# Kernel tuning notes

Measured on AMD Instinct MI355X. Metric: run time of the kernel, lower is better.

The kernel has to match this reference:

```python
import jax, jax.numpy as jnp
import numpy as np

N_NODES = 20000
DIM = 128
N_EDGES = 500000
BATCH = 16384
EPS = 1e-6  # torch.nn.PairwiseDistance default eps


def setup_inputs() -> dict:
    key = jax.random.key(0)
    k = jax.random.split(key, 8)
    edges = jax.random.randint(k[0], (2, N_EDGES), 0, N_NODES, dtype=jnp.int64 if jax.config.jax_enable_x64 else jnp.int32)
    nodes_p_star = jnp.sort(jax.random.randint(k[1], (BATCH,), 0, N_NODES))
    nodes_p = jnp.sort(jax.random.randint(k[2], (BATCH,), 0, N_NODES))
    # learned parameters, init in [-1, 1) as in the torch module
    beta_p = 2.0 * jax.random.uniform(k[3], (N_NODES,), dtype=jnp.float32) - 1.0
    beta_p_star = 2.0 * jax.random.uniform(k[4], (N_NODES,), dtype=jnp.float32) - 1.0
    p = 2.0 * jax.random.uniform(k[5], (N_NODES, DIM), dtype=jnp.float32) - 1.0
    p_star = 2.0 * jax.random.uniform(k[6], (N_NODES, DIM), dtype=jnp.float32) - 1.0
    return {
        "edges": edges,
        "nodes_p_star": nodes_p_star,
        "nodes_p": nodes_p,
        "beta_p": beta_p,
        "beta_p_star": beta_p_star,
        "p": p,
        "p_star": p_star,
    }


def reference(edges, nodes_p_star, nodes_p, beta_p, beta_p_star, p, p_star):
    # ---- link term: sum over observed edges of (beta - dist) ----
    beta_pair = beta_p_star[edges[0]] + beta_p[edges[1]]  # [E]
    diff = p[edges[0]] - p_star[edges[1]]                 # [E, D]
    # torch PairwiseDistance adds eps to the difference before the norm
    z_dist = jnp.sqrt(jnp.sum((diff + EPS) ** 2, axis=-1))
    link_term = jnp.sum(beta_pair - z_dist)

    # ---- non-link term: triu-masked sum of exp(beta - cdist) ----
    bps = beta_p_star[nodes_p_star]   # [Ns]
    bp = beta_p[nodes_p]              # [Np]
    ps = p_star[nodes_p_star]         # [Ns, D]
    pp = p[nodes_p]                   # [Np, D]
    beta_mat = bps[None, :] + bp[:, None]          # [Np, Ns]
    # cdist(ps, pp) -> [Ns, Np] via Gram trick
    sq = (jnp.sum(ps * ps, axis=-1)[:, None]
          + jnp.sum(pp * pp, axis=-1)[None, :]
          - 2.0 * jnp.einsum('nd,md->nm', ps, pp))
    dist_mat = jnp.sqrt(jnp.maximum(sq, 0.0))      # [Ns, Np]
    intensity = jnp.exp(beta_mat.T - dist_mat)     # [Ns, Np]
    non_link = jnp.sum(jnp.triu(intensity, k=1))

    return -(link_term - non_link)
```

## Files before the change

kernel.cpp:

```cpp
#include <hip/hip_runtime.h>

#define N_NODES 20000
#define DIM 128
#define N_EDGES 500000
#define BATCH 16384
#define EPS 1e-6f
#define L2E 1.4426950408889634f

typedef _Float16 half8 __attribute__((ext_vector_type(8)));
typedef _Float16 half4_t __attribute__((ext_vector_type(4)));
typedef float f32x4 __attribute__((ext_vector_type(4)));

__device__ __forceinline__ float fast_sqrtf(float x) {
#if __has_builtin(__builtin_amdgcn_sqrtf)
    return __builtin_amdgcn_sqrtf(x);
#else
    return sqrtf(x);
#endif
}
__device__ __forceinline__ float fast_exp2f(float x) {
#if __has_builtin(__builtin_amdgcn_exp2f)
    return __builtin_amdgcn_exp2f(x);
#else
    return exp2f(x);
#endif
}

#define NB_TILE 8256
#define N_BLK   512

#define OFF_PGEMM 0
#define OFF_CTR   16384
#define OFF_PSH   33280
#define OFF_PPH   4227584
#define OFF_N2S   8421888
#define OFF_N2P   8487424
#define OFF_BPS   8552960
#define OFF_BP    8618496
#define OFF_END   8684032

__global__ __launch_bounds__(256) void prep_kernel(
    const float* __restrict__ p, const float* __restrict__ p_star,
    const float* __restrict__ beta_p, const float* __restrict__ beta_ps,
    const int* __restrict__ nodes_ps, const int* __restrict__ nodes_p,
    _Float16* __restrict__ Ah, float* __restrict__ n2A, float* __restrict__ bA2,
    _Float16* __restrict__ Bh, float* __restrict__ n2B, float* __restrict__ bB2,
    unsigned* __restrict__ ctr)
{
    if (blockIdx.x == 0 && threadIdx.x == 0) *ctr = 0u;
    const int bx = blockIdx.x;
    const int g = threadIdx.x & 31;
    const int r8 = threadIdx.x >> 5;
    const bool isA = bx < 2048;
    const int row = (isA ? bx : bx - 2048) * 8 + r8;
    const int id = isA ? nodes_ps[row] : nodes_p[row];
    const float* src = isA ? p_star : p;
    float4 v = ((const float4*)(src + (size_t)id * DIM))[g];
    half4_t o;
    o[0] = (_Float16)v.x; o[1] = (_Float16)v.y; o[2] = (_Float16)v.z; o[3] = (_Float16)v.w;
    const int h = g >> 4;
    const int pc = ((g >> 1) & 7) ^ (row & 7);
    _Float16* dst = isA ? Ah : Bh;
    *(half4_t*)(dst + (size_t)row * DIM + (((h << 3) | pc) << 3) + (g & 1) * 4) = o;
    float nrm = v.x * v.x + v.y * v.y + v.z * v.z + v.w * v.w;
    #pragma unroll
    for (int m = 16; m >= 1; m >>= 1) nrm += __shfl_xor(nrm, m, 32);
    if (g == 0) {
        if (isA) { n2A[row] = nrm; bA2[row] = L2E * beta_ps[id]; }
        else     { n2B[row] = nrm; bB2[row] = L2E * beta_p[id]; }
    }
}

__device__ __forceinline__ void tile_of(int t, int& i0, int& j0, bool& diag) {
    const int by = t / 129;
    const int bx = t - by * 129;
    const int len = 128 - by;
    int ti, tj;
    if (bx < len) { ti = by; tj = by + bx; }
    else          { ti = 127 - by; tj = 127 - (bx - len); }
    i0 = ti << 7; j0 = tj << 7; diag = (ti == tj);
}

#define STAGE_ARR(BASE0, GSRC, LDSOFF)                                             \
    {                                                                              \
        _Pragma("unroll")                                                          \
        for (int u = 0; u < 4; ++u) {                                              \
            const int g8 = u * 8 + w;                                   \
            const int h = g8 >> 4, rg = g8 & 15;                                   \
            __builtin_amdgcn_global_load_lds(                                      \
                (const __attribute__((address_space(1))) void*)((GSRC) +           \
                    (((size_t)((BASE0) + rg * 8 + (lane >> 3))) << 8)              \
                    + (h << 7) + ((lane & 7) << 4)),                               \
                (__attribute__((address_space(3))) void*)(lds + (LDSOFF)           \
                    + h * 16384 + rg * 1024), 16, 0, 0);                           \
        }                                                                          \
    }

#define STAGE_A(I0) STAGE_ARR(I0, gA, 0)
#define STAGE_B(J0) STAGE_ARR(J0, gB, 32768)

__global__ __launch_bounds__(512, 4) void main_kernel(
    const _Float16* __restrict__ Ag, const _Float16* __restrict__ Bg,
    const float* __restrict__ n2A, const float* __restrict__ n2B,
    const float* __restrict__ bA2, const float* __restrict__ bB2,
    const int* __restrict__ edges,
    const float* __restrict__ beta_p, const float* __restrict__ beta_ps,
    const float* __restrict__ pf, const float* __restrict__ psf,
    float* __restrict__ pgemm, unsigned* __restrict__ ctr,
    float* __restrict__ out)
{
    __shared__ __align__(16) _Float16 sm16[32768];
    __shared__ float smr[8];
    __shared__ int lastflag;

    const int b = blockIdx.x;
    const int tid = threadIdx.x;
    const int lane = tid & 63;
    const int w = tid >> 6;
    const int wm = w & 3;
    const int wn = w >> 2;
    const int quad = lane >> 4;
    const int lr = lane & 15;
    const int k7 = lr & 7;

    auto* lds = (__attribute__((address_space(3))) char*)sm16;
    const auto* gA = (const __attribute__((address_space(1))) char*)Ag;
    const auto* gB = (const __attribute__((address_space(1))) char*)Bg;

    float lsum = 0.f;

    const int start = b * 16 + (b < 64 ? b : 64);
    const int tend = start + 16 + (b < 64 ? 1 : 0);

    int t = start;
    int i0, j0; bool diag;
    tile_of(t, i0, j0, diag);
    STAGE_A(i0)
    STAGE_B(j0)
    __syncthreads();

    for (;;) {
        int cls = 0;
        if (diag) cls = (wn == 0) ? (wm >= 2 ? 2 : 1) : (wm >= 2 ? 1 : 0);

        f32x4 acc[2][4] = {};
        if (cls != 2) {
            #pragma unroll
            for (int ks = 0; ks < 4; ++ks) {
                const int h = ks >> 1;
                const int pc = (((ks & 1) << 2) | quad) ^ k7;
                const int hb = h * 8192;
                half8 af[2], bf[4];
                #pragma unroll
                for (int u = 0; u < 2; ++u)
                    af[u] = *(const half8*)&sm16[hb + (wm * 32 + u * 16 + lr) * 64 + pc * 8];
                #pragma unroll
                for (int v = 0; v < 4; ++v)
                    bf[v] = *(const half8*)&sm16[16384 + hb + (wn * 64 + v * 16 + lr) * 64 + pc * 8];
                #pragma unroll
                for (int mi = 0; mi < 2; ++mi)
                    #pragma unroll
                    for (int ni = 0; ni < 4; ++ni)
                        acc[mi][ni] = __builtin_amdgcn_mfma_f32_16x16x32_f16(
                            af[mi], bf[ni], acc[mi][ni], 0, 0, 0);
            }
        }

        const int ilo = i0 + wm * 32, jlo = j0 + wn * 64;
        const int tcur = t;
        __syncthreads();

        t += 1;
        const bool more = (t < tend);
        if (more) {
            const int pi0 = i0;
            tile_of(t, i0, j0, diag);
            if (i0 != pi0) STAGE_A(i0)
            STAGE_B(j0)
        }

        #pragma unroll
        for (int tt = 0; tt < 2; ++tt) {
            int e = tcur * 64 + w * 8 + quad * 2 + tt;
            if (e < N_EDGES) {
                int e0 = edges[e];
                int e1 = edges[N_EDGES + e];
                const float* ar = pf + (size_t)e0 * DIM + lr * 8;
                const float* br = psf + (size_t)e1 * DIM + lr * 8;
                f32x4 a0 = *(const f32x4*)ar;   f32x4 a1 = *(const f32x4*)(ar + 4);
                f32x4 b0 = *(const f32x4*)br;   f32x4 b1 = *(const f32x4*)(br + 4);
                float eb2 = (lr == 0) ? (beta_ps[e0] + beta_p[e1]) : 0.f;
                float s = 0.f;
                #pragma unroll
                for (int k = 0; k < 4; ++k) { float d = a0[k] - b0[k] + EPS; s = fmaf(d, d, s); }
                #pragma unroll
                for (int k = 0; k < 4; ++k) { float d = a1[k] - b1[k] + EPS; s = fmaf(d, d, s); }
                #pragma unroll
                for (int m = 8; m >= 1; m >>= 1) s += __shfl_xor(s, m, 16);
                if (lr == 0) lsum -= eb2 - fast_sqrtf(s);
            }
        }

        if (cls != 2) {
            f32x4 n2i[2], bi[2];
            #pragma unroll
            for (int mi = 0; mi < 2; ++mi) {
                n2i[mi] = *(const f32x4*)&n2A[ilo + mi * 16 + quad * 4];
                bi[mi]  = *(const f32x4*)&bA2[ilo + mi * 16 + quad * 4];
            }
            float n2j[4], bj[4];
            #pragma unroll
            for (int ni = 0; ni < 4; ++ni) {
                n2j[ni] = n2B[jlo + ni * 16 + lr];
                bj[ni]  = bB2[jlo + ni * 16 + lr];
            }

            if (cls == 0) {
                #pragma unroll
                for (int mi = 0; mi < 2; ++mi)
                    #pragma unroll
                    for (int ni = 0; ni < 4; ++ni) {
                        f32x4 d = acc[mi][ni];
                        f32x4 ttv = n2i[mi] + n2j[ni];
                        f32x4 sq = d * -2.0f + ttv;
                        f32x4 bs = bi[mi] + bj[ni];
                        #pragma unroll
                        for (int r = 0; r < 4; ++r) {
                            float m0 = fmaxf(sq[r], 0.f);
                            float arg = fmaf(fast_sqrtf(m0), -L2E, bs[r]);
                            lsum += fast_exp2f(arg);
                        }
                    }
            } else {
                #pragma unroll
                for (int mi = 0; mi < 2; ++mi)
                    #pragma unroll
                    for (int ni = 0; ni < 4; ++ni) {
                        f32x4 d = acc[mi][ni];
                        f32x4 ttv = n2i[mi] + n2j[ni];
                        f32x4 sq = d * -2.0f + ttv;
                        f32x4 bs = bi[mi] + bj[ni];
                        #pragma unroll
                        for (int r = 0; r < 4; ++r) {
                            int ig = ilo + mi * 16 + quad * 4 + r;
                            int jg = jlo + ni * 16 + lr;
                            float m0 = fmaxf(sq[r], 0.f);
                            float arg = fmaf(fast_sqrtf(m0), -L2E, bs[r]);
                            float ex = fast_exp2f(arg);
                            if (jg > ig) lsum += ex;
                        }
                    }
            }
        }

        if (!more) break;
        __syncthreads();
    }

    #pragma unroll
    for (int m = 32; m >= 1; m >>= 1) lsum += __shfl_xor(lsum, m, 64);
    if (lane == 0) smr[w] = lsum;
    __syncthreads();
    if (tid == 0) {
        float s = 0.f;
        #pragma unroll
        for (int i = 0; i < 8; ++i) s += smr[i];
        pgemm[b] = s;
        unsigned prev = __hip_atomic_fetch_add(ctr, 1u, __ATOMIC_ACQ_REL,
                                               __HIP_MEMORY_SCOPE_AGENT);
        lastflag = (prev == N_BLK - 1) ? 1 : 0;
    }
    __syncthreads();

    if (lastflag) {
        float s = __hip_atomic_load(&pgemm[tid], __ATOMIC_RELAXED,
                                    __HIP_MEMORY_SCOPE_AGENT);
        #pragma unroll
        for (int m = 32; m >= 1; m >>= 1) s += __shfl_xor(s, m, 64);
        if (lane == 0) smr[w] = s;
        __syncthreads();
        if (tid == 0) {
            float tsum = 0.f;
            #pragma unroll
            for (int i = 0; i < 8; ++i) tsum += smr[i];
            out[0] = tsum;
        }
    }
}

extern "C" void kernel_launch(void* const* d_in, const int* in_sizes, int n_in,
                              void* d_out, int out_size, void* d_ws, size_t ws_size,
                              hipStream_t stream) {
    const int* edges = (const int*)d_in[0];
    const int* nodes_p_star = (const int*)d_in[1];
    const int* nodes_p = (const int*)d_in[2];
    const float* beta_p = (const float*)d_in[3];
    const float* beta_p_star = (const float*)d_in[4];
    const float* p = (const float*)d_in[5];
    const float* p_star = (const float*)d_in[6];

    char* ws = (char*)d_ws;
    float* pgemm = (float*)(ws + OFF_PGEMM);
    unsigned* ctr = (unsigned*)(ws + OFF_CTR);
    _Float16* psh = (_Float16*)(ws + OFF_PSH);
    _Float16* pph = (_Float16*)(ws + OFF_PPH);
    float* n2s = (float*)(ws + OFF_N2S);
    float* n2p = (float*)(ws + OFF_N2P);
    float* bps2 = (float*)(ws + OFF_BPS);
    float* bp2 = (float*)(ws + OFF_BP);

    prep_kernel<<<4096, 256, 0, stream>>>(
        p, p_star, beta_p, beta_p_star, nodes_p_star, nodes_p,
        psh, n2s, bps2, pph, n2p, bp2, ctr);

    main_kernel<<<N_BLK, 512, 0, stream>>>(
        psh, pph, n2s, n2p, bps2, bp2,
        edges, beta_p, beta_p_star, p, p_star,
        pgemm, ctr, (float*)d_out);
}
```

Baseline: 194.4 us.

## Halve B tile to 64 columns, raise occupancy, and pack epilogue math in float2

Each 128x128 tile is split into two 128x64 half-steps. This halves the B staging in LDS (48KB instead of 64KB) and the per-wave accumulator count, and lets launch bounds rise from 4 to 6 blocks per CU. Each step now processes half as many edges, so the total edge coverage is unchanged. The exp/sqrt epilogue is rewritten to use two-wide float vectors with a vector accumulator, aiming at packed FP32 ops. In exchange there are more barriers and more B reloads per A tile, and each wave has less MFMA work to hide latency.

```diff
diff --git a/kernel.cpp b/kernel.cpp
--- a/kernel.cpp
+++ b/kernel.cpp
@@ -10,6 +10,7 @@
 typedef _Float16 half8 __attribute__((ext_vector_type(8)));
 typedef _Float16 half4_t __attribute__((ext_vector_type(4)));
 typedef float f32x4 __attribute__((ext_vector_type(4)));
+typedef float f32x2 __attribute__((ext_vector_type(2)));
 
 __device__ __forceinline__ float fast_sqrtf(float x) {
 #if __has_builtin(__builtin_amdgcn_sqrtf)
@@ -27,6 +28,7 @@
 }
 
 #define NB_TILE 8256
+#define NB_STEP 16512
 #define N_BLK   512
 
 #define OFF_PGEMM 0
@@ -71,35 +73,47 @@
     }
 }
 
-__device__ __forceinline__ void tile_of(int t, int& i0, int& j0, bool& diag) {
+__device__ __forceinline__ void tile_of(int t, int& i0, int& tjb, bool& diag) {
     const int by = t / 129;
     const int bx = t - by * 129;
     const int len = 128 - by;
     int ti, tj;
     if (bx < len) { ti = by; tj = by + bx; }
     else          { ti = 127 - by; tj = 127 - (bx - len); }
-    i0 = ti << 7; j0 = tj << 7; diag = (ti == tj);
-}
-
-#define STAGE_ARR(BASE0, GSRC, LDSOFF)                                             \
+    i0 = ti << 7; tjb = tj << 7; diag = (ti == tj);
+}
+
+#define STAGE_A(I0)                                                                \
     {                                                                              \
         _Pragma("unroll")                                                          \
         for (int u = 0; u < 4; ++u) {                                              \
             const int g8 = u * 8 + w;                                   \
             const int h = g8 >> 4, rg = g8 & 15;                                   \
             __builtin_amdgcn_global_load_lds(                                      \
-                (const __attribute__((address_space(1))) void*)((GSRC) +           \
-                    (((size_t)((BASE0) + rg * 8 + (lane >> 3))) << 8)              \
+                (const __attribute__((address_space(1))) void*)(gA +               \
+                    (((size_t)((I0) + rg * 8 + (lane >> 3))) << 8)                 \
                     + (h << 7) + ((lane & 7) << 4)),                               \
-                (__attribute__((address_space(3))) void*)(lds + (LDSOFF)           \
+                (__attribute__((address_space(3))) void*)(lds                      \
                     + h * 16384 + rg * 1024), 16, 0, 0);                           \
         }                                                                          \
     }
 
-#define STAGE_A(I0) STAGE_ARR(I0, gA, 0)
-#define STAGE_B(J0) STAGE_ARR(J0, gB, 32768)
-
-__global__ __launch_bounds__(512, 4) void main_kernel(
+#define STAGE_B(JB)                                                                \
+    {                                                                              \
+        _Pragma("unroll")                                                          \
+        for (int u = 0; u < 2; ++u) {                                              \
+            const int g8 = u * 8 + w;                                   \
+            const int h = g8 >> 3, rg = g8 & 7;                                    \
+            __builtin_amdgcn_global_load_lds(                                      \
+                (const __attribute__((address_space(1))) void*)(gB +               \
+                    (((size_t)((JB) + rg * 8 + (lane >> 3))) << 8)                 \
+                    + (h << 7) + ((lane & 7) << 4)),                               \
+                (__attribute__((address_space(3))) void*)(lds + 32768              \
+                    + h * 8192 + rg * 1024), 16, 0, 0);                            \
+        }                                                                          \
+    }
+
+__global__ __launch_bounds__(512, 6) void main_kernel(
     const _Float16* __restrict__ Ag, const _Float16* __restrict__ Bg,
     const float* __restrict__ n2A, const float* __restrict__ n2B,
     const float* __restrict__ bA2, const float* __restrict__ bB2,
@@ -109,7 +123,7 @@
     float* __restrict__ pgemm, unsigned* __restrict__ ctr,
     float* __restrict__ out)
 {
-    __shared__ __align__(16) _Float16 sm16[32768];
+    __shared__ __align__(16) _Float16 sm16[24576];
     __shared__ float smr[8];
     __shared__ int lastflag;
 
@@ -128,60 +142,65 @@
     const auto* gB = (const __attribute__((address_space(1))) char*)Bg;
 
     float lsum = 0.f;
-
-    const int start = b * 16 + (b < 64 ? b : 64);
-    const int tend = start + 16 + (b < 64 ? 1 : 0);
-
-    int t = start;
-    int i0, j0; bool diag;
-    tile_of(t, i0, j0, diag);
-    STAGE_A(i0)
-    STAGE_B(j0)
+    f32x2 lacc = {0.f, 0.f};
+
+    const int start = b * 32 + (b < 128 ? b : 128);
+    const int tend = start + 32 + (b < 128 ? 1 : 0);
+
+    int s = start;
+    int i0, tjb; bool diag;
+    {
+        tile_of(s >> 1, i0, tjb, diag);
+        const int hb = s & 1;
+        STAGE_A(i0)
+        STAGE_B(tjb + hb * 64)
+    }
     __syncthreads();
 
     for (;;) {
+        const int hb = s & 1;
         int cls = 0;
-        if (diag) cls = (wn == 0) ? (wm >= 2 ? 2 : 1) : (wm >= 2 ? 1 : 0);
-
-        f32x4 acc[2][4] = {};
+        if (diag) { const int cj = hb * 2 + wn; cls = (cj > wm) ? 0 : (cj == wm ? 1 : 2); }
+
+        f32x4 acc[2][2] = {};
         if (cls != 2) {
             #pragma unroll
             for (int ks = 0; ks < 4; ++ks) {
                 const int h = ks >> 1;
                 const int pc = (((ks & 1) << 2) | quad) ^ k7;
-                const int hb = h * 8192;
-                half8 af[2], bf[4];
+                half8 af[2], bf[2];
                 #pragma unroll
                 for (int u = 0; u < 2; ++u)
-                    af[u] = *(const half8*)&sm16[hb + (wm * 32 + u * 16 + lr) * 64 + pc * 8];
-                #pragma unroll
-                for (int v = 0; v < 4; ++v)
-                    bf[v] = *(const half8*)&sm16[16384 + hb + (wn * 64 + v * 16 + lr) * 64 + pc * 8];
+                    af[u] = *(const half8*)&sm16[h * 8192 + (wm * 32 + u * 16 + lr) * 64 + pc * 8];
+                #pragma unroll
+                for (int v = 0; v < 2; ++v)
+                    bf[v] = *(const half8*)&sm16[16384 + h * 4096 + (wn * 32 + v * 16 + lr) * 64 + pc * 8];
                 #pragma unroll
                 for (int mi = 0; mi < 2; ++mi)
                     #pragma unroll
-                    for (int ni = 0; ni < 4; ++ni)
+                    for (int ni = 0; ni < 2; ++ni)
                         acc[mi][ni] = __builtin_amdgcn_mfma_f32_16x16x32_f16(
                             af[mi], bf[ni], acc[mi][ni], 0, 0, 0);
             }
         }
 
-        const int ilo = i0 + wm * 32, jlo = j0 + wn * 64;
-        const int tcur = t;
+        const int ilo = i0 + wm * 32;
+        const int jlo = tjb + hb * 64 + wn * 32;
+        const int scur = s;
         __syncthreads();
 
-        t += 1;
-        const bool more = (t < tend);
+        s += 1;
+        const bool more = (s < tend);
         if (more) {
             const int pi0 = i0;
-            tile_of(t, i0, j0, diag);
+            tile_of(s >> 1, i0, tjb, diag);
             if (i0 != pi0) STAGE_A(i0)
-            STAGE_B(j0)
+            STAGE_B(tjb + (s & 1) * 64)
         }
 
         #pragma unroll
-        for (int tt = 0; tt < 2; ++tt) {
-            int e = tcur * 64 + w * 8 + quad * 2 + tt;
+        for (int tt = 0; tt < 1; ++tt) {
+            int e = scur * 32 + w * 4 + quad;
             if (e < N_EDGES) {
                 int e0 = edges[e];
                 int e1 = edges[N_EDGES + e];
@@ -190,14 +209,14 @@
                 f32x4 a0 = *(const f32x4*)ar;   f32x4 a1 = *(const f32x4*)(ar + 4);
                 f32x4 b0 = *(const f32x4*)br;   f32x4 b1 = *(const f32x4*)(br + 4);
                 float eb2 = (lr == 0) ? (beta_ps[e0] + beta_p[e1]) : 0.f;
-                float s = 0.f;
-                #pragma unroll
-                for (int k = 0; k < 4; ++k) { float d = a0[k] - b0[k] + EPS; s = fmaf(d, d, s); }
-                #pragma unroll
-                for (int k = 0; k < 4; ++k) { float d = a1[k] - b1[k] + EPS; s = fmaf(d, d, s); }
-                #pragma unroll
-                for (int m = 8; m >= 1; m >>= 1) s += __shfl_xor(s, m, 16);
-                if (lr == 0) lsum -= eb2 - fast_sqrtf(s);
+                float ssum = 0.f;
+                #pragma unroll
+                for (int k = 0; k < 4; ++k) { float d = a0[k] - b0[k] + EPS; ssum = fmaf(d, d, ssum); }
+                #pragma unroll
+                for (int k = 0; k < 4; ++k) { float d = a1[k] - b1[k] + EPS; ssum = fmaf(d, d, ssum); }
+                #pragma unroll
+                for (int m = 8; m >= 1; m >>= 1) ssum += __shfl_xor(ssum, m, 16);
+                if (lr == 0) lsum -= eb2 - fast_sqrtf(ssum);
             }
         }
 
@@ -208,64 +227,59 @@
                 n2i[mi] = *(const f32x4*)&n2A[ilo + mi * 16 + quad * 4];
                 bi[mi]  = *(const f32x4*)&bA2[ilo + mi * 16 + quad * 4];
             }
-            float n2j[4], bj[4];
-            #pragma unroll
-            for (int ni = 0; ni < 4; ++ni) {
+            float n2j[2], bj[2];
+            #pragma unroll
+            for (int ni = 0; ni < 2; ++ni) {
                 n2j[ni] = n2B[jlo + ni * 16 + lr];
                 bj[ni]  = bB2[jlo + ni * 16 + lr];
             }
 
-            if (cls == 0) {
-                #pragma unroll
-                for (int mi = 0; mi < 2; ++mi)
+            #pragma unroll
+            for (int mi = 0; mi < 2; ++mi)
+                #pragma unroll
+                for (int ni = 0; ni < 2; ++ni) {
+                    const f32x4 d = acc[mi][ni];
                     #pragma unroll
-                    for (int ni = 0; ni < 4; ++ni) {
-                        f32x4 d = acc[mi][ni];
-                        f32x4 ttv = n2i[mi] + n2j[ni];
-                        f32x4 sq = d * -2.0f + ttv;
-                        f32x4 bs = bi[mi] + bj[ni];
-                        #pragma unroll
-                        for (int r = 0; r < 4; ++r) {
-                            float m0 = fmaxf(sq[r], 0.f);
-                            float arg = fmaf(fast_sqrtf(m0), -L2E, bs[r]);
-                            lsum += fast_exp2f(arg);
+                    for (int pr = 0; pr < 2; ++pr) {
+                        f32x2 d2 = { d[2 * pr], d[2 * pr + 1] };
+                        f32x2 t2 = { n2i[mi][2 * pr] + n2j[ni], n2i[mi][2 * pr + 1] + n2j[ni] };
+                        f32x2 sq2 = d2 * -2.0f + t2;
+                        f32x2 z2 = { 0.f, 0.f };
+                        f32x2 mx2 = __builtin_elementwise_max(sq2, z2);
+                        float s0 = fast_sqrtf(mx2[0]);
+                        float s1 = fast_sqrtf(mx2[1]);
+                        f32x2 bs2 = { bi[mi][2 * pr] + bj[ni], bi[mi][2 * pr + 1] + bj[ni] };
+                        f32x2 sr2 = { s0, s1 };
+                        f32x2 ar2 = sr2 * -L2E + bs2;
+                        float e0 = fast_exp2f(ar2[0]);
+                        float e1 = fast_exp2f(ar2[1]);
+                        if (cls == 0) {
+                            f32x2 e2 = { e0, e1 };
+                            lacc += e2;
+                        } else {
+                            const int ig0 = ilo + mi * 16 + quad * 4 + 2 * pr;
+                            const int jg = jlo + ni * 16 + lr;
+                            if (jg > ig0)     lacc[0] += e0;
+                            if (jg > ig0 + 1) lacc[1] += e1;
                         }
                     }
-            } else {
-                #pragma unroll
-                for (int mi = 0; mi < 2; ++mi)
-                    #pragma unroll
-                    for (int ni = 0; ni < 4; ++ni) {
-                        f32x4 d = acc[mi][ni];
-                        f32x4 ttv = n2i[mi] + n2j[ni];
-                        f32x4 sq = d * -2.0f + ttv;
-                        f32x4 bs = bi[mi] + bj[ni];
-                        #pragma unroll
-                        for (int r = 0; r < 4; ++r) {
-                            int ig = ilo + mi * 16 + quad * 4 + r;
-                            int jg = jlo + ni * 16 + lr;
-                            float m0 = fmaxf(sq[r], 0.f);
-                            float arg = fmaf(fast_sqrtf(m0), -L2E, bs[r]);
-                            float ex = fast_exp2f(arg);
-                            if (jg > ig) lsum += ex;
-                        }
-                    }
-            }
+                }
         }
 
         if (!more) break;
         __syncthreads();
     }
 
+    lsum += lacc[0] + lacc[1];
     #pragma unroll
     for (int m = 32; m >= 1; m >>= 1) lsum += __shfl_xor(lsum, m, 64);
     if (lane == 0) smr[w] = lsum;
     __syncthreads();
     if (tid == 0) {
-        float s = 0.f;
+        float ssum = 0.f;
         #pragma unroll
-        for (int i = 0; i < 8; ++i) s += smr[i];
-        pgemm[b] = s;
+        for (int i = 0; i < 8; ++i) ssum += smr[i];
+        pgemm[b] = ssum;
         unsigned prev = __hip_atomic_fetch_add(ctr, 1u, __ATOMIC_ACQ_REL,
                                                __HIP_MEMORY_SCOPE_AGENT);
         lastflag = (prev == N_BLK - 1) ? 1 : 0;
@@ -273,11 +287,11 @@
     __syncthreads();
 
     if (lastflag) {
-        float s = __hip_atomic_load(&pgemm[tid], __ATOMIC_RELAXED,
+        float v = __hip_atomic_load(&pgemm[tid], __ATOMIC_RELAXED,
                                     __HIP_MEMORY_SCOPE_AGENT);
         #pragma unroll
-        for (int m = 32; m >= 1; m >>= 1) s += __shfl_xor(s, m, 64);
-        if (lane == 0) smr[w] = s;
+        for (int m = 32; m >= 1; m >>= 1) v += __shfl_xor(v, m, 64);
+        if (lane == 0) smr[w] = v;
         __syncthreads();
         if (tid == 0) {
             float tsum = 0.f;
```

Result: slower. 208.4 us (+7.3%).

## Convert full embedding tables to fp16 and prefetch edge gathers before MFMA

Applied to the files above, without the earlier changes.

The prep kernel now also converts the full p and p_star tables to fp16, and when the workspace is large enough the edge term gathers half8 rows instead of fp32, halving the gather bytes. Edge indices and rows are loaded at the top of each tile iteration so their latency overlaps the MFMA work. Row norms and betas for the A tile are hoisted and reloaded only when the A tile changes, and the block-to-tile-run mapping is interleaved by b&7. The cost is an extra pass over both 20000x128 tables in prep, fp16 rounding in the link-distance term, and more live registers during the MFMA loop.

```diff
diff --git a/kernel.cpp b/kernel.cpp
--- a/kernel.cpp
+++ b/kernel.cpp
@@ -37,7 +37,9 @@
 #define OFF_N2P   8487424
 #define OFF_BPS   8552960
 #define OFF_BP    8618496
-#define OFF_END   8684032
+#define OFF_P16   8684032
+#define OFF_PS16  13804032
+#define OFF_END   18924032
 
 __global__ __launch_bounds__(256) void prep_kernel(
     const float* __restrict__ p, const float* __restrict__ p_star,
@@ -45,29 +47,41 @@
     const int* __restrict__ nodes_ps, const int* __restrict__ nodes_p,
     _Float16* __restrict__ Ah, float* __restrict__ n2A, float* __restrict__ bA2,
     _Float16* __restrict__ Bh, float* __restrict__ n2B, float* __restrict__ bB2,
+    _Float16* __restrict__ p16, _Float16* __restrict__ ps16,
     unsigned* __restrict__ ctr)
 {
     if (blockIdx.x == 0 && threadIdx.x == 0) *ctr = 0u;
     const int bx = blockIdx.x;
     const int g = threadIdx.x & 31;
     const int r8 = threadIdx.x >> 5;
-    const bool isA = bx < 2048;
-    const int row = (isA ? bx : bx - 2048) * 8 + r8;
-    const int id = isA ? nodes_ps[row] : nodes_p[row];
-    const float* src = isA ? p_star : p;
-    float4 v = ((const float4*)(src + (size_t)id * DIM))[g];
-    half4_t o;
-    o[0] = (_Float16)v.x; o[1] = (_Float16)v.y; o[2] = (_Float16)v.z; o[3] = (_Float16)v.w;
-    const int h = g >> 4;
-    const int pc = ((g >> 1) & 7) ^ (row & 7);
-    _Float16* dst = isA ? Ah : Bh;
-    *(half4_t*)(dst + (size_t)row * DIM + (((h << 3) | pc) << 3) + (g & 1) * 4) = o;
-    float nrm = v.x * v.x + v.y * v.y + v.z * v.z + v.w * v.w;
-    #pragma unroll
-    for (int m = 16; m >= 1; m >>= 1) nrm += __shfl_xor(nrm, m, 32);
-    if (g == 0) {
-        if (isA) { n2A[row] = nrm; bA2[row] = L2E * beta_ps[id]; }
-        else     { n2B[row] = nrm; bB2[row] = L2E * beta_p[id]; }
+    if (bx < 4096) {
+        const bool isA = bx < 2048;
+        const int row = (isA ? bx : bx - 2048) * 8 + r8;
+        const int id = isA ? nodes_ps[row] : nodes_p[row];
+        const float* src = isA ? p_star : p;
+        float4 v = ((const float4*)(src + (size_t)id * DIM))[g];
+        half4_t o;
+        o[0] = (_Float16)v.x; o[1] = (_Float16)v.y; o[2] = (_Float16)v.z; o[3] = (_Float16)v.w;
+        const int h = g >> 4;
+        const int pc = ((g >> 1) & 7) ^ (row & 7);
+        _Float16* dst = isA ? Ah : Bh;
+        *(half4_t*)(dst + (size_t)row * DIM + (((h << 3) | pc) << 3) + (g & 1) * 4) = o;
+        float nrm = v.x * v.x + v.y * v.y + v.z * v.z + v.w * v.w;
+        #pragma unroll
+        for (int m = 16; m >= 1; m >>= 1) nrm += __shfl_xor(nrm, m, 32);
+        if (g == 0) {
+            if (isA) { n2A[row] = nrm; bA2[row] = L2E * beta_ps[id]; }
+            else     { n2B[row] = nrm; bB2[row] = L2E * beta_p[id]; }
+        }
+    } else {
+        const bool isP = bx < 6596;
+        const int row = (isP ? bx - 4096 : bx - 6596) * 8 + r8;
+        const float* src = isP ? p : p_star;
+        _Float16* dst = isP ? p16 : ps16;
+        float4 v = ((const float4*)(src + (size_t)row * DIM))[g];
+        half4_t o;
+        o[0] = (_Float16)v.x; o[1] = (_Float16)v.y; o[2] = (_Float16)v.z; o[3] = (_Float16)v.w;
+        *(half4_t*)(dst + (size_t)row * DIM + g * 4) = o;
     }
 }
 
@@ -81,7 +95,7 @@
     i0 = ti << 7; j0 = tj << 7; diag = (ti == tj);
 }
 
-#define STAGE_ARR(BASE0, GSRC, LDSOFF)                                             \
+#define STAGE_ARR(BASE0, GSRC, LOFF)                                               \
     {                                                                              \
         _Pragma("unroll")                                                          \
         for (int u = 0; u < 4; ++u) {                                              \
@@ -91,7 +105,7 @@
                 (const __attribute__((address_space(1))) void*)((GSRC) +           \
                     (((size_t)((BASE0) + rg * 8 + (lane >> 3))) << 8)              \
                     + (h << 7) + ((lane & 7) << 4)),                               \
-                (__attribute__((address_space(3))) void*)(lds + (LDSOFF)           \
+                (__attribute__((address_space(3))) void*)(lds + (LOFF)             \
                     + h * 16384 + rg * 1024), 16, 0, 0);                           \
         }                                                                          \
     }
@@ -105,7 +119,8 @@
     const float* __restrict__ bA2, const float* __restrict__ bB2,
     const int* __restrict__ edges,
     const float* __restrict__ beta_p, const float* __restrict__ beta_ps,
-    const float* __restrict__ pf, const float* __restrict__ psf,
+    const _Float16* __restrict__ p16, const _Float16* __restrict__ ps16,
+    const float* __restrict__ pf, const float* __restrict__ psf, int use16,
     float* __restrict__ pgemm, unsigned* __restrict__ ctr,
     float* __restrict__ out)
 {
@@ -129,17 +144,53 @@
 
     float lsum = 0.f;
 
-    const int start = b * 16 + (b < 64 ? b : 64);
-    const int tend = start + 16 + (b < 64 ? 1 : 0);
+    const int run = (b & 7) * 64 + (b >> 3);
+    const int start = run * 16 + (run < 64 ? run : 64);
+    const int tend = start + 16 + (run < 64 ? 1 : 0);
 
     int t = start;
     int i0, j0; bool diag;
     tile_of(t, i0, j0, diag);
     STAGE_A(i0)
     STAGE_B(j0)
+
+    f32x4 n2i[2], bi[2];
+    {
+        const int ilo = i0 + wm * 32;
+        #pragma unroll
+        for (int mi = 0; mi < 2; ++mi) {
+            n2i[mi] = *(const f32x4*)&n2A[ilo + mi * 16 + quad * 4];
+            bi[mi]  = *(const f32x4*)&bA2[ilo + mi * 16 + quad * 4];
+        }
+    }
     __syncthreads();
 
     for (;;) {
+        half8 ea[2], eb[2];
+        f32x4 fa0[2], fa1[2], fb0[2], fb1[2];
+        float ebeta[2];
+        bool ev[2];
+        #pragma unroll
+        for (int tt = 0; tt < 2; ++tt) {
+            const int e = t * 64 + w * 8 + quad * 2 + tt;
+            ev[tt] = (e < N_EDGES);
+            ebeta[tt] = 0.f;
+            if (ev[tt]) {
+                int e0 = edges[e];
+                int e1 = edges[N_EDGES + e];
+                if (use16) {
+                    ea[tt] = *(const half8*)(p16 + (size_t)e0 * DIM + lr * 8);
+                    eb[tt] = *(const half8*)(ps16 + (size_t)e1 * DIM + lr * 8);
+                } else {
+                    const float* ar = pf + (size_t)e0 * DIM + lr * 8;
+                    const float* br = psf + (size_t)e1 * DIM + lr * 8;
+                    fa0[tt] = *(const f32x4*)ar;  fa1[tt] = *(const f32x4*)(ar + 4);
+                    fb0[tt] = *(const f32x4*)br;  fb1[tt] = *(const f32x4*)(br + 4);
+                }
+                if (lr == 0) ebeta[tt] = beta_ps[e0] + beta_p[e1];
+            }
+        }
+
         int cls = 0;
         if (diag) cls = (wn == 0) ? (wm >= 2 ? 2 : 1) : (wm >= 2 ? 1 : 0);
 
@@ -149,14 +200,13 @@
             for (int ks = 0; ks < 4; ++ks) {
                 const int h = ks >> 1;
                 const int pc = (((ks & 1) << 2) | quad) ^ k7;
-                const int hb = h * 8192;
                 half8 af[2], bf[4];
                 #pragma unroll
                 for (int u = 0; u < 2; ++u)
-                    af[u] = *(const half8*)&sm16[hb + (wm * 32 + u * 16 + lr) * 64 + pc * 8];
+                    af[u] = *(const half8*)&sm16[h * 8192 + (wm * 32 + u * 16 + lr) * 64 + pc * 8];
                 #pragma unroll
                 for (int v = 0; v < 4; ++v)
-                    bf[v] = *(const half8*)&sm16[16384 + hb + (wn * 64 + v * 16 + lr) * 64 + pc * 8];
+                    bf[v] = *(const half8*)&sm16[16384 + h * 8192 + (wn * 64 + v * 16 + lr) * 64 + pc * 8];
                 #pragma unroll
                 for (int mi = 0; mi < 2; ++mi)
                     #pragma unroll
@@ -166,48 +216,45 @@
             }
         }
 
-        const int ilo = i0 + wm * 32, jlo = j0 + wn * 64;
+        const int ilo = i0 + wm * 32;
+        const int jlo = j0 + wn * 64;
         const int tcur = t;
         __syncthreads();
 
         t += 1;
         const bool more = (t < tend);
+        bool achg = false;
         if (more) {
             const int pi0 = i0;
             tile_of(t, i0, j0, diag);
-            if (i0 != pi0) STAGE_A(i0)
+            achg = (i0 != pi0);
+            if (achg) STAGE_A(i0)
             STAGE_B(j0)
         }
 
         #pragma unroll
         for (int tt = 0; tt < 2; ++tt) {
-            int e = tcur * 64 + w * 8 + quad * 2 + tt;
-            if (e < N_EDGES) {
-                int e0 = edges[e];
-                int e1 = edges[N_EDGES + e];
-                const float* ar = pf + (size_t)e0 * DIM + lr * 8;
-                const float* br = psf + (size_t)e1 * DIM + lr * 8;
-                f32x4 a0 = *(const f32x4*)ar;   f32x4 a1 = *(const f32x4*)(ar + 4);
-                f32x4 b0 = *(const f32x4*)br;   f32x4 b1 = *(const f32x4*)(br + 4);
-                float eb2 = (lr == 0) ? (beta_ps[e0] + beta_p[e1]) : 0.f;
+            if (ev[tt]) {
                 float s = 0.f;
-                #pragma unroll
-                for (int k = 0; k < 4; ++k) { float d = a0[k] - b0[k] + EPS; s = fmaf(d, d, s); }
-                #pragma unroll
-                for (int k = 0; k < 4; ++k) { float d = a1[k] - b1[k] + EPS; s = fmaf(d, d, s); }
+                if (use16) {
+                    #pragma unroll
+                    for (int k = 0; k < 8; ++k) {
+                        float d = (float)ea[tt][k] - (float)eb[tt][k] + EPS;
+                        s = fmaf(d, d, s);
+                    }
+                } else {
+                    #pragma unroll
+                    for (int k = 0; k < 4; ++k) { float d = fa0[tt][k] - fb0[tt][k] + EPS; s = fmaf(d, d, s); }
+                    #pragma unroll
+                    for (int k = 0; k < 4; ++k) { float d = fa1[tt][k] - fb1[tt][k] + EPS; s = fmaf(d, d, s); }
+                }
                 #pragma unroll
                 for (int m = 8; m >= 1; m >>= 1) s += __shfl_xor(s, m, 16);
-                if (lr == 0) lsum -= eb2 - fast_sqrtf(s);
+                if (lr == 0) lsum -= ebeta[tt] - fast_sqrtf(s);
             }
         }
 
         if (cls != 2) {
-            f32x4 n2i[2], bi[2];
-            #pragma unroll
-            for (int mi = 0; mi < 2; ++mi) {
-                n2i[mi] = *(const f32x4*)&n2A[ilo + mi * 16 + quad * 4];
-                bi[mi]  = *(const f32x4*)&bA2[ilo + mi * 16 + quad * 4];
-            }
             float n2j[4], bj[4];
             #pragma unroll
             for (int ni = 0; ni < 4; ++ni) {
@@ -221,13 +268,11 @@
                     #pragma unroll
                     for (int ni = 0; ni < 4; ++ni) {
                         f32x4 d = acc[mi][ni];
-                        f32x4 ttv = n2i[mi] + n2j[ni];
-                        f32x4 sq = d * -2.0f + ttv;
-                        f32x4 bs = bi[mi] + bj[ni];
                         #pragma unroll
                         for (int r = 0; r < 4; ++r) {
-                            float m0 = fmaxf(sq[r], 0.f);
-                            float arg = fmaf(fast_sqrtf(m0), -L2E, bs[r]);
+                            float ttv = n2i[mi][r] + n2j[ni];
+                            float sq = fmaxf(fmaf(d[r], -2.f, ttv), 0.f);
+                            float arg = fmaf(fast_sqrtf(sq), -L2E, bi[mi][r] + bj[ni]);
                             lsum += fast_exp2f(arg);
                         }
                     }
@@ -237,15 +282,13 @@
                     #pragma unroll
                     for (int ni = 0; ni < 4; ++ni) {
                         f32x4 d = acc[mi][ni];
-                        f32x4 ttv = n2i[mi] + n2j[ni];
-                        f32x4 sq = d * -2.0f + ttv;
-                        f32x4 bs = bi[mi] + bj[ni];
                         #pragma unroll
                         for (int r = 0; r < 4; ++r) {
                             int ig = ilo + mi * 16 + quad * 4 + r;
                             int jg = jlo + ni * 16 + lr;
-                            float m0 = fmaxf(sq[r], 0.f);
-                            float arg = fmaf(fast_sqrtf(m0), -L2E, bs[r]);
+                            float ttv = n2i[mi][r] + n2j[ni];
+                            float sq = fmaxf(fmaf(d[r], -2.f, ttv), 0.f);
+                            float arg = fmaf(fast_sqrtf(sq), -L2E, bi[mi][r] + bj[ni]);
                             float ex = fast_exp2f(arg);
                             if (jg > ig) lsum += ex;
                         }
@@ -254,6 +297,14 @@
         }
 
         if (!more) break;
+        if (achg) {
+            const int nilo = i0 + wm * 32;
+            #pragma unroll
+            for (int mi = 0; mi < 2; ++mi) {
+                n2i[mi] = *(const f32x4*)&n2A[nilo + mi * 16 + quad * 4];
+                bi[mi]  = *(const f32x4*)&bA2[nilo + mi * 16 + quad * 4];
+            }
+        }
         __syncthreads();
     }
 
@@ -262,10 +313,10 @@
     if (lane == 0) smr[w] = lsum;
     __syncthreads();
     if (tid == 0) {
-        float s = 0.f;
-        #pragma unroll
-        for (int i = 0; i < 8; ++i) s += smr[i];
-        pgemm[b] = s;
+        float ssum = 0.f;
+        #pragma unroll
+        for (int i = 0; i < 8; ++i) ssum += smr[i];
+        pgemm[b] = ssum;
         unsigned prev = __hip_atomic_fetch_add(ctr, 1u, __ATOMIC_ACQ_REL,
                                                __HIP_MEMORY_SCOPE_AGENT);
         lastflag = (prev == N_BLK - 1) ? 1 : 0;
@@ -273,11 +324,11 @@
     __syncthreads();
 
     if (lastflag) {
-        float s = __hip_atomic_load(&pgemm[tid], __ATOMIC_RELAXED,
+        float v = __hip_atomic_load(&pgemm[tid], __ATOMIC_RELAXED,
                                     __HIP_MEMORY_SCOPE_AGENT);
         #pragma unroll
-        for (int m = 32; m >= 1; m >>= 1) s += __shfl_xor(s, m, 64);
-        if (lane == 0) smr[w] = s;
+        for (int m = 32; m >= 1; m >>= 1) v += __shfl_xor(v, m, 64);
+        if (lane == 0) smr[w] = v;
         __syncthreads();
         if (tid == 0) {
             float tsum = 0.f;
@@ -308,13 +359,18 @@
     float* n2p = (float*)(ws + OFF_N2P);
     float* bps2 = (float*)(ws + OFF_BPS);
     float* bp2 = (float*)(ws + OFF_BP);
-
-    prep_kernel<<<4096, 256, 0, stream>>>(
+    _Float16* p16 = (_Float16*)(ws + OFF_P16);
+    _Float16* ps16 = (_Float16*)(ws + OFF_PS16);
+
+    const int use16 = (ws_size >= (size_t)OFF_END) ? 1 : 0;
+    const int prep_grid = use16 ? 9096 : 4096;
+
+    prep_kernel<<<prep_grid, 256, 0, stream>>>(
         p, p_star, beta_p, beta_p_star, nodes_p_star, nodes_p,
-        psh, n2s, bps2, pph, n2p, bp2, ctr);
+        psh, n2s, bps2, pph, n2p, bp2, p16, ps16, ctr);
 
     main_kernel<<<N_BLK, 512, 0, stream>>>(
         psh, pph, n2s, n2p, bps2, bp2,
-        edges, beta_p, beta_p_star, p, p_star,
+        edges, beta_p, beta_p_star, p16, ps16, p, p_star, use16,
         pgemm, ctr, (float*)d_out);
 }
```

After: 300.1 us. 54.4% more time.
